# Performance work log

Hardware: AMD Instinct MI355X
Metric: run time of the kernel (lower is better)

## Reference

```python
import jax, jax.numpy as jnp
import numpy as np

H = 4  # n_heads in nn.MultiheadAttention
LN_EPS = 1e-5


def _mha_seq1(x_q, x_kv, in_w, in_b, out_w, out_b):
    """torch nn.MultiheadAttention with batch_first and seq_len=1 on q and kv.
    x_q, x_kv: [B, F]. in_w: [3F, F] (packed q/k/v), out_w: [F, F].
    With a single kv position, softmax over the kv axis is identically 1,
    so the output equals out_proj(v); we still compute scores/softmax so the
    math (and zero grads to Wq/Wk) matches torch exactly.
    """
    B, F = x_q.shape
    dh = F // H
    wq, wk, wv = jnp.split(in_w, 3, axis=0)
    bq, bk, bv = jnp.split(in_b, 3, axis=0)
    q = (x_q @ wq.T + bq).reshape(B, H, dh)
    k = (x_kv @ wk.T + bk).reshape(B, H, dh)
    v = (x_kv @ wv.T + bv).reshape(B, H, dh)
    s = jnp.einsum('bhd,bhd->bh', q, k) / jnp.sqrt(jnp.asarray(dh, x_q.dtype))
    w = jax.nn.softmax(s[..., None], axis=-1)  # [B, H, 1] == 1
    o = (w * v).reshape(B, F)
    return o @ out_w.T + out_b


def _layer_norm(x, g, b):
    mu = jnp.mean(x, axis=-1, keepdims=True)
    var = jnp.mean(jnp.square(x - mu), axis=-1, keepdims=True)
    return (x - mu) * jax.lax.rsqrt(var + LN_EPS) * g + b


def setup_inputs() -> dict:
    key = jax.random.key(0)
    B, GD, TD, F = 16384, 1024, 1024, 2048
    ks = jax.random.split(key, 20)
    s = 0.02  # weight init scale
    return {
        'graph_feat': jax.random.normal(ks[0], (B, GD), jnp.float32),
        'temporal_feat': jax.random.normal(ks[1], (B, TD), jnp.float32),
        'gp_w': jax.random.normal(ks[2], (F, GD), jnp.float32) * s,
        'gp_b': jax.random.normal(ks[3], (F,), jnp.float32) * s,
        'tp_w': jax.random.normal(ks[4], (F, TD), jnp.float32) * s,
        'tp_b': jax.random.normal(ks[5], (F,), jnp.float32) * s,
        'in1_w': jax.random.normal(ks[6], (3 * F, F), jnp.float32) * s,
        'in1_b': jax.random.normal(ks[7], (3 * F,), jnp.float32) * s,
        'out1_w': jax.random.normal(ks[8], (F, F), jnp.float32) * s,
        'out1_b': jax.random.normal(ks[9], (F,), jnp.float32) * s,
        'in2_w': jax.random.normal(ks[10], (3 * F, F), jnp.float32) * s,
        'in2_b': jax.random.normal(ks[11], (3 * F,), jnp.float32) * s,
        'out2_w': jax.random.normal(ks[12], (F, F), jnp.float32) * s,
        'out2_b': jax.random.normal(ks[13], (F,), jnp.float32) * s,
        'gate_w': jax.random.normal(ks[14], (F, 2 * F), jnp.float32) * s,
        'gate_b': jax.random.normal(ks[15], (F,), jnp.float32) * s,
        'ln_g': jnp.ones((F,), jnp.float32),
        'ln_b': jnp.zeros((F,), jnp.float32),
        'lin_w': jax.random.normal(ks[16], (F, F), jnp.float32) * s,
        'lin_b': jax.random.normal(ks[17], (F,), jnp.float32) * s,
    }


def reference(graph_feat, temporal_feat, gp_w, gp_b, tp_w, tp_b,
              in1_w, in1_b, out1_w, out1_b, in2_w, in2_b, out2_w, out2_b,
              gate_w, gate_b, ln_g, ln_b, lin_w, lin_b):
    g = graph_feat @ gp_w.T + gp_b          # [B, F]
    t = temporal_feat @ tp_w.T + tp_b       # [B, F]
    attn1 = _mha_seq1(g, t, in1_w, in1_b, out1_w, out1_b)  # cross1(g, t, t)
    attn2 = _mha_seq1(t, g, in2_w, in2_b, out2_w, out2_b)  # cross2(t, g, g)
    cross = attn1 + attn2
    gate = jax.nn.sigmoid(jnp.concatenate([g, cross], axis=-1) @ gate_w.T + gate_b)
    fused = gate * g + (1.0 - gate) * cross
    fused = _layer_norm(fused + g, ln_g, ln_b)
    return fused @ lin_w.T + lin_b
```

## Files before the change

### kernel.cpp

```cpp
#include <hip/hip_runtime.h>
#include <stdint.h>

typedef __attribute__((ext_vector_type(8))) short short8;
typedef __attribute__((ext_vector_type(4))) float f32x4;

__device__ __forceinline__ unsigned short f2bf(float f) {
  union { float f; uint32_t u; } v; v.f = f;
  uint32_t u = v.u;
  u += 0x7FFF + ((u >> 16) & 1);
  return (unsigned short)(u >> 16);
}
__device__ __forceinline__ float bf2f(unsigned short h) {
  union { uint32_t u; float f; } v; v.u = ((uint32_t)h) << 16;
  return v.f;
}

__global__ void conv_kernel(const float* __restrict__ in,
                            unsigned short* __restrict__ out, int n) {
  long i = ((long)blockIdx.x * blockDim.x + threadIdx.x) * 8;
  if (i >= n) return;
  float4 a = *(const float4*)(in + i);
  float4 b = *(const float4*)(in + i + 4);
  short8 s;
  s[0] = (short)f2bf(a.x); s[1] = (short)f2bf(a.y);
  s[2] = (short)f2bf(a.z); s[3] = (short)f2bf(a.w);
  s[4] = (short)f2bf(b.x); s[5] = (short)f2bf(b.y);
  s[6] = (short)f2bf(b.z); s[7] = (short)f2bf(b.w);
  *(short8*)(out + i) = s;
}

__global__ void convcat_kernel(const float* __restrict__ in,
                               unsigned short* __restrict__ out,
                               int colbase, int n) {
  long i = ((long)blockIdx.x * blockDim.x + threadIdx.x) * 8;
  if (i >= n) return;
  float4 a = *(const float4*)(in + i);
  float4 b = *(const float4*)(in + i + 4);
  short8 s;
  s[0] = (short)f2bf(a.x); s[1] = (short)f2bf(a.y);
  s[2] = (short)f2bf(a.z); s[3] = (short)f2bf(a.w);
  s[4] = (short)f2bf(b.x); s[5] = (short)f2bf(b.y);
  s[6] = (short)f2bf(b.z); s[7] = (short)f2bf(b.w);
  long row = i >> 10, col = i & 1023;
  *(short8*)(out + row * 2048 + colbase + col) = s;
}

__global__ void convs_kernel(const float* __restrict__ in,
                             const float* __restrict__ scale,
                             unsigned short* __restrict__ out, int n) {
  long i = ((long)blockIdx.x * blockDim.x + threadIdx.x) * 8;
  if (i >= n) return;
  short8 s;
#pragma unroll
  for (int j = 0; j < 8; ++j)
    s[j] = (short)f2bf(in[i + j] * scale[(i + j) & 2047]);
  *(short8*)(out + i) = s;
}

__global__ void tconv_kernel(const float* __restrict__ in, int R, int C,
                             unsigned short* __restrict__ out) {
  __shared__ float tile[32][33];
  int c0 = blockIdx.x * 32, r0 = blockIdx.y * 32;
  int tx = threadIdx.x, ty = threadIdx.y;
#pragma unroll
  for (int i = 0; i < 32; i += 8)
    tile[ty + i][tx] = in[(long)(r0 + ty + i) * C + c0 + tx];
  __syncthreads();
#pragma unroll
  for (int i = 0; i < 32; i += 8)
    out[(long)(c0 + ty + i) * R + r0 + tx] = f2bf(tile[tx][ty + i]);
}

enum { CE_PLAIN = 0, CE_WT = 1, CE_ACC = 2 };

template <int CE>
__global__ __launch_bounds__(256)
void compose_kernel(const unsigned short* __restrict__ A, int lda,
                    const unsigned short* __restrict__ W, int ldw,
                    unsigned short* C, int ldc,
                    unsigned short* Ct, long ctoff,
                    int K, int nmt,
                    int pairBase, long aoff, long woff, long coff) {
  constexpr int BK = 32;
  __shared__ unsigned short sA[128 * BK];
  __shared__ unsigned short sB[128 * BK];
  const int tid  = threadIdx.x;
  const int lane = tid & 63;
  const int wave = tid >> 6;
  const int wr = (wave >> 1) * 64;
  const int wc = (wave & 1) * 64;

  int bid = blockIdx.x;
  if (bid >= pairBase) {
    bid -= pairBase;
    A += aoff; W += woff; C += coff; Ct += ctoff;
  }
  const long tileM = (long)(bid % nmt) * 128;
  const long tileN = (long)(bid / nmt) * 128;

  const unsigned short* gA = A + (tileM + (tid >> 2)) * (long)lda + (tid & 3) * 8;
  const unsigned short* gB = W + (tileN + (tid >> 2)) * (long)ldw + (tid & 3) * 8;
  unsigned short* lA = sA + wave * 512;
  unsigned short* lB = sB + wave * 512;

  f32x4 acc[4][4] = {};
  const int fr = lane & 15;
  const int kb = (lane >> 4) * 8;

  for (int k0 = 0; k0 < K; k0 += BK) {
    __builtin_amdgcn_global_load_lds(
        (const __attribute__((address_space(1))) void*)(gA + k0),
        (__attribute__((address_space(3))) void*)(lA), 16, 0, 0);
    __builtin_amdgcn_global_load_lds(
        (const __attribute__((address_space(1))) void*)(gA + k0 + 64 * (long)lda),
        (__attribute__((address_space(3))) void*)(lA + 2048), 16, 0, 0);
    __builtin_amdgcn_global_load_lds(
        (const __attribute__((address_space(1))) void*)(gB + k0),
        (__attribute__((address_space(3))) void*)(lB), 16, 0, 0);
    __builtin_amdgcn_global_load_lds(
        (const __attribute__((address_space(1))) void*)(gB + k0 + 64 * (long)ldw),
        (__attribute__((address_space(3))) void*)(lB + 2048), 16, 0, 0);
    __syncthreads();

    short8 aF[4], bF[4];
#pragma unroll
    for (int m = 0; m < 4; ++m)
      aF[m] = *(const short8*)&sA[(wr + m * 16 + fr) * BK + kb];
#pragma unroll
    for (int n = 0; n < 4; ++n)
      bF[n] = *(const short8*)&sB[(wc + n * 16 + fr) * BK + kb];
#pragma unroll
    for (int m = 0; m < 4; ++m)
#pragma unroll
      for (int n = 0; n < 4; ++n)
        acc[m][n] = __builtin_amdgcn_mfma_f32_16x16x32_bf16(aF[m], bF[n], acc[m][n], 0, 0, 0);
    __syncthreads();
  }

  const int cr = (lane >> 4) * 4;
  const int cc = lane & 15;
#pragma unroll
  for (int m = 0; m < 4; ++m) {
    long r0 = tileM + wr + m * 16 + cr;
#pragma unroll
    for (int n = 0; n < 4; ++n) {
      long c = tileN + wc + n * 16 + cc;
#pragma unroll
      for (int r = 0; r < 4; ++r) {
        long idx = (r0 + r) * (long)ldc + c;
        float v = acc[m][n][r];
        if constexpr (CE == CE_ACC) v += bf2f(C[idx]);
        unsigned short bv = f2bf(v);
        C[idx] = bv;
        if constexpr (CE == CE_WT) Ct[c * 2048 + (r0 + r)] = bv;
      }
    }
  }
}

enum { EPI_BIAS = 0, EPI_LNF32 = 4 };

#define VMW(N) asm volatile("s_waitcnt vmcnt(" #N ")" ::: "memory")
#define SBAR() __builtin_amdgcn_s_barrier()
#define SCB() __builtin_amdgcn_sched_barrier(0)

#define STG(D, OP, HALF, PTR, LD8)                                            \
  { char* lp_ = (char*)smem + ((D)*65536 + (OP)*32768 + (HALF)*16384 + w*2048); \
    __builtin_amdgcn_global_load_lds(                                         \
        (const __attribute__((address_space(1))) void*)(PTR),                 \
        (__attribute__((address_space(3))) void*)lp_, 16, 0, 0);              \
    __builtin_amdgcn_global_load_lds(                                         \
        (const __attribute__((address_space(1))) void*)((PTR) + (LD8)),       \
        (__attribute__((address_space(3))) void*)(lp_ + 1024), 16, 0, 0);     \
    (PTR) += 64; }
#define NOSTG ((void)0)

#define RDA(D, KK) ((KK) ? ((D) ? pA11 : pA01) : ((D) ? pA10 : pA00))
#define RDB(D, KK) ((KK) ? ((D) ? pB11 : pB01) : ((D) ? pB10 : pB00))

template <int EPI, int SWZ>
__global__ __launch_bounds__(512, 2)
void gemm8p_kernel(const unsigned short* __restrict__ A, int lda,
                   const unsigned short* __restrict__ W, int ldw,
                   int K, int ldc, int nmt,
                   const float* __restrict__ bias,
                   const float* __restrict__ bias2,
                   const float2* __restrict__ stats,
                   void* Cv) {
  __shared__ unsigned short smem[65536];

  const int tid = threadIdx.x, lane = tid & 63, w = tid >> 6;
  const int wm = w >> 2, wn = w & 3;

  int bid = blockIdx.x;
  int mt, nt;
  if (SWZ) {
    const int xcd = bid & 7, seq = bid >> 3;
    nt = seq >> 3;
    mt = xcd * 8 + (seq & 7);
  } else {
    mt = bid % nmt;
    nt = bid / nmt;
  }
  const long tileM = (long)mt * 256, tileN = (long)nt * 256;

  const int sRow = w * 16 + (lane >> 3);
  const int sCol = (((lane & 7) ^ ((lane >> 3) & 7)) * 8);
  const unsigned short* pSA0 = A + (tileM + sRow) * (long)lda + sCol;
  const unsigned short* pSA1 = pSA0 + 128 * (long)lda;
  const unsigned short* pSB0 = W + (tileN + sRow) * (long)ldw + sCol;
  const unsigned short* pSB1 = pSB0 + 128 * (long)ldw;
  const long lda8 = 8 * (long)lda, ldw8 = 8 * (long)ldw;

  const int fr = lane & 15, kc = lane >> 4, l7 = lane & 7;
  const char* pA00 = (const char*)smem + (wm * 16 + fr) * 128 + ((kc) ^ l7) * 16;
  const char* pA01 = (const char*)smem + (wm * 16 + fr) * 128 + ((4 + kc) ^ l7) * 16;
  const char* pA10 = pA00 + 65536;
  const char* pA11 = pA01 + 65536;
  const char* pB00 = (const char*)smem + 32768 + (wn * 16 + fr) * 128 + ((kc) ^ l7) * 16;
  const char* pB01 = (const char*)smem + 32768 + (wn * 16 + fr) * 128 + ((4 + kc) ^ l7) * 16;
  const char* pB10 = pB00 + 65536;
  const char* pB11 = pB01 + 65536;

  f32x4 acc[8][4] = {};
  short8 aH[4][2];
  short8 bqS[2][2][2];

#define MPHASE(D, MQ, LB, STGX)                                               \
  {                                                                           \
    _Pragma("unroll") for (int mi = 0; mi < 2; ++mi) {                        \
      aH[mi][0] = *(const short8*)(RDA(D, 0) + (MQ)*16384 + mi * 4096);       \
      aH[mi][1] = *(const short8*)(RDA(D, 1) + (MQ)*16384 + mi * 4096);       \
    }                                                                         \
    if (LB) {                                                                 \
      _Pragma("unroll") for (int q = 0; q < 2; ++q)                           \
      _Pragma("unroll") for (int ni = 0; ni < 2; ++ni) {                      \
        bqS[q][ni][0] = *(const short8*)(RDB(D, 0) + q * 16384 + ni * 8192);  \
        bqS[q][ni][1] = *(const short8*)(RDB(D, 1) + q * 16384 + ni * 8192);  \
      }                                                                       \
    }                                                                         \
    _Pragma("unroll") for (int mi = 2; mi < 4; ++mi) {                        \
      aH[mi][0] = *(const short8*)(RDA(D, 0) + (MQ)*16384 + mi * 4096);       \
      aH[mi][1] = *(const short8*)(RDA(D, 1) + (MQ)*16384 + mi * 4096);       \
    }                                                                         \
    STGX;                                                                     \
    __builtin_amdgcn_s_setprio(1);                                            \
    _Pragma("unroll") for (int mi = 0; mi < 4; ++mi)                          \
    _Pragma("unroll") for (int n = 0; n < 4; ++n) {                           \
      acc[(MQ)*4+mi][n] = __builtin_amdgcn_mfma_f32_16x16x32_bf16(            \
          aH[mi][0], bqS[n >> 1][n & 1][0], acc[(MQ)*4+mi][n], 0, 0, 0);      \
      acc[(MQ)*4+mi][n] = __builtin_amdgcn_mfma_f32_16x16x32_bf16(            \
          aH[mi][1], bqS[n >> 1][n & 1][1], acc[(MQ)*4+mi][n], 0, 0, 0);      \
    }                                                                         \
    __builtin_amdgcn_s_setprio(0);                                            \
    SCB();                                                                    \
  }

  STG(0, 0, 0, pSA0, lda8);
  STG(0, 1, 0, pSB0, ldw8);
  STG(0, 1, 1, pSB1, ldw8);
  STG(0, 0, 1, pSA1, lda8);
  STG(1, 0, 0, pSA0, lda8);
  STG(1, 1, 0, pSB0, ldw8);
  STG(1, 1, 1, pSB1, ldw8);
  VMW(8);
  SBAR();

  const int NIT = K / 128;
  for (int it = 0; it < NIT - 1; ++it) {
    MPHASE(0, 0, 1, STG(1, 0, 1, pSA1, lda8));            VMW(8); SBAR();
    MPHASE(0, 1, 0, STG(0, 0, 0, pSA0, lda8);
                    STG(0, 1, 0, pSB0, ldw8);
                    STG(0, 1, 1, pSB1, ldw8));            VMW(8); SBAR();
    MPHASE(1, 0, 1, STG(0, 0, 1, pSA1, lda8));            VMW(8); SBAR();
    MPHASE(1, 1, 0, STG(1, 0, 0, pSA0, lda8);
                    STG(1, 1, 0, pSB0, ldw8);
                    STG(1, 1, 1, pSB1, ldw8));            VMW(8); SBAR();
  }
  {
    MPHASE(0, 0, 1, STG(1, 0, 1, pSA1, lda8)); VMW(8); SBAR();
    MPHASE(0, 1, 0, NOSTG);                    VMW(2); SBAR();
    MPHASE(1, 0, 1, NOSTG);                    VMW(0); SBAR();
    MPHASE(1, 1, 0, NOSTG);
  }
#undef MPHASE

  const int cr = (lane >> 4) * 4;
  const int cc = lane & 15;
#pragma unroll
  for (int m = 0; m < 8; ++m) {
    long rr = tileM + (m >> 2) * 128 + (m & 3) * 32 + wm * 16 + cr;
#pragma unroll
    for (int n = 0; n < 4; ++n) {
      long c = tileN + (n >> 1) * 128 + (n & 1) * 64 + wn * 16 + cc;
      float b1 = bias ? bias[c] : 0.0f;
      float b2 = bias2 ? bias2[c] : 0.0f;
#pragma unroll
      for (int r = 0; r < 4; ++r) {
        long row = rr + r;
        long idx = row * (long)ldc + c;
        float v = acc[m][n][r];
        if constexpr (EPI == EPI_BIAS) {
          ((unsigned short*)Cv)[idx] = f2bf(v + b1 + b2);
        }
        if constexpr (EPI == EPI_LNF32) {
          float2 st = stats[row];
          ((float*)Cv)[idx] = v * st.y - st.y * st.x * b1 + b2;
        }
      }
    }
  }
}

__global__ __launch_bounds__(256) void fusestats_kernel(
    const unsigned short* __restrict__ CL, const unsigned short* __restrict__ G,
    unsigned short* __restrict__ PL, float2* __restrict__ stats) {
  const int row = blockIdx.x;
  const int t = threadIdx.x, lane = t & 63, wave = t >> 6;
  short8 xc = *(const short8*)&CL[(long)row * 4096 + t * 8];
  short8 xl = *(const short8*)&CL[(long)row * 4096 + 2048 + t * 8];
  short8 xg = *(const short8*)&G[(long)row * 2048 + t * 8];
  short8 o8;
  float s = 0.f, s2 = 0.f;
#pragma unroll
  for (int j = 0; j < 8; ++j) {
    float cv = bf2f((unsigned short)xc[j]);
    float lv = bf2f((unsigned short)xl[j]);
    float gv = bf2f((unsigned short)xg[j]);
    float gt = 1.0f / (1.0f + expf(-lv));
    unsigned short pb = f2bf(gt * gv + (1.0f - gt) * cv + gv);
    o8[j] = (short)pb;
    float x = bf2f(pb);
    s += x; s2 += x * x;
  }
  *(short8*)(PL + (long)row * 2048 + t * 8) = o8;
#pragma unroll
  for (int off = 1; off < 64; off <<= 1) {
    s  += __shfl_xor(s, off);
    s2 += __shfl_xor(s2, off);
  }
  __shared__ float red[8];
  if (lane == 0) { red[wave] = s; red[4 + wave] = s2; }
  __syncthreads();
  if (t == 0) {
    float ts  = red[0] + red[1] + red[2] + red[3];
    float ts2 = red[4] + red[5] + red[6] + red[7];
    float mean = ts * (1.0f / 2048.0f);
    float var  = ts2 * (1.0f / 2048.0f) - mean * mean;
    stats[row] = make_float2(mean, rsqrtf(var + 1e-5f));
  }
}

__device__ __forceinline__ float blkRed(float s, float* red, int lane, int wave) {
#pragma unroll
  for (int off = 1; off < 64; off <<= 1) s += __shfl_xor(s, off);
  if (lane == 0) red[wave] = s;
  __syncthreads();
  return red[0] + red[1] + red[2] + red[3];
}

__global__ __launch_bounds__(256) void biascompP_kernel(
    const unsigned short* __restrict__ wO1b, const unsigned short* __restrict__ wO2b,
    const unsigned short* __restrict__ Wc1, const unsigned short* __restrict__ Wc2,
    const float* __restrict__ bv1, const float* __restrict__ bv2,
    const float* __restrict__ tpb, const float* __restrict__ gpb,
    const float* __restrict__ o1b, const float* __restrict__ o2b,
    float* __restrict__ bcV) {
  __shared__ float red[4];
  int c = blockIdx.x, t = threadIdx.x, lane = t & 63, wave = t >> 6;
  int k = t * 8;
  float s = 0.f;
  short8 a1 = *(const short8*)(wO1b + (long)c * 2048 + k);
  short8 a2 = *(const short8*)(wO2b + (long)c * 2048 + k);
  short8 a3 = *(const short8*)(Wc1 + (long)c * 2048 + k);
  short8 a4 = *(const short8*)(Wc2 + (long)c * 2048 + k);
#pragma unroll
  for (int j = 0; j < 8; ++j)
    s += bf2f((unsigned short)a1[j]) * bv1[k + j]
       + bf2f((unsigned short)a2[j]) * bv2[k + j]
       + bf2f((unsigned short)a3[j]) * tpb[k + j]
       + bf2f((unsigned short)a4[j]) * gpb[k + j];
  float tot = blkRed(s, red, lane, wave);
  if (t == 0) bcV[c] = tot + o1b[c] + o2b[c];
}

__global__ __launch_bounds__(256) void bgateP_kernel(
    const float* __restrict__ gate_w, const float* __restrict__ gate_b,
    const float* __restrict__ gpb, const float* __restrict__ bcV,
    float* __restrict__ bgateV) {
  __shared__ float red[4];
  int n = blockIdx.x, t = threadIdx.x, lane = t & 63, wave = t >> 6;
  const float* row = gate_w + (long)n * 4096;
  float s = 0.f;
  int k = t * 8;
#pragma unroll
  for (int j = 0; j < 8; ++j)
    s += row[k + j] * gpb[k + j] + row[2048 + k + j] * bcV[k + j];
  float tot = blkRed(s, red, lane, wave);
  if (t == 0) bgateV[n] = tot + gate_b[n];
}

__global__ __launch_bounds__(256) void uvP_kernel(
    const unsigned short* __restrict__ wlinp, const float* __restrict__ lin_w,
    const float* __restrict__ ln_beta, const float* __restrict__ lin_b,
    float* __restrict__ uV, float* __restrict__ vV) {
  __shared__ float redu[4], redv[4];
  int n = blockIdx.x, t = threadIdx.x, lane = t & 63, wave = t >> 6;
  int k = t * 8;
  short8 a1 = *(const short8*)(wlinp + (long)n * 2048 + k);
  float u = 0.f, v = 0.f;
#pragma unroll
  for (int j = 0; j < 8; ++j) {
    u += bf2f((unsigned short)a1[j]);
    v += ln_beta[k + j] * lin_w[(long)n * 2048 + k + j];
  }
#pragma unroll
  for (int off = 1; off < 64; off <<= 1) {
    u += __shfl_xor(u, off);
    v += __shfl_xor(v, off);
  }
  if (lane == 0) { redu[wave] = u; redv[wave] = v; }
  __syncthreads();
  if (t == 0) {
    uV[n] = redu[0] + redu[1] + redu[2] + redu[3];
    vV[n] = redv[0] + redv[1] + redv[2] + redv[3] + lin_b[n];
  }
}

extern "C" void kernel_launch(void* const* d_in, const int* in_sizes, int n_in,
                              void* d_out, int out_size, void* d_ws, size_t ws_size,
                              hipStream_t stream) {
  const float* graph    = (const float*)d_in[0];
  const float* temporal = (const float*)d_in[1];
  const float* gp_w  = (const float*)d_in[2];
  const float* gp_b  = (const float*)d_in[3];
  const float* tp_w  = (const float*)d_in[4];
  const float* tp_b  = (const float*)d_in[5];
  const float* in1_w = (const float*)d_in[6];
  const float* in1_b = (const float*)d_in[7];
  const float* out1_w = (const float*)d_in[8];
  const float* out1_b = (const float*)d_in[9];
  const float* in2_w = (const float*)d_in[10];
  const float* in2_b = (const float*)d_in[11];
  const float* out2_w = (const float*)d_in[12];
  const float* out2_b = (const float*)d_in[13];
  const float* gate_w = (const float*)d_in[14];
  const float* gate_b = (const float*)d_in[15];
  const float* ln_g  = (const float*)d_in[16];
  const float* ln_b  = (const float*)d_in[17];
  const float* lin_w = (const float*)d_in[18];
  const float* lin_b = (const float*)d_in[19];

  const int Bm = 16384, F = 2048, GD = 1024;
  const long BF = (long)Bm * F, FF = (long)F * F, FG = (long)F * GD;

  unsigned short* TG   = (unsigned short*)d_ws;
  unsigned short* PL   = TG;
  unsigned short* Gbuf = TG + BF;
  unsigned short* wLIN = Gbuf + BF;
  unsigned short* wGP  = wLIN + FF;
  unsigned short* Wcg  = wGP + FG;
  unsigned short* Wcross = Wcg;
  unsigned short* Wgate  = Wcg + FF;
  float* bc2V   = (float*)(Wcg + 2 * FF);
  float* uV     = bc2V + 2 * F;
  float* vV     = uV + F;
  float2* stats = (float2*)(vV + F);

  unsigned short* DO      = (unsigned short*)d_out;
  unsigned short* wv1T    = DO;
  unsigned short* wv2T    = wv1T + FF;
  unsigned short* tpT     = wv2T + FF;
  unsigned short* gpT     = tpT + FG;
  unsigned short* Wc1     = gpT + FG;
  unsigned short* Wc2     = Wc1 + FF;
  unsigned short* wO1b    = Wc2 + FF;
  unsigned short* wO2b    = wO1b + FF;
  unsigned short* wGATEb  = wO2b + FF;
  unsigned short* WcrossT = wGATEb + 2 * FF;
  unsigned short* CL      = DO;

  auto conv = [&](const float* src, unsigned short* dst, long n) {
    conv_kernel<<<dim3((unsigned)(n / 8 / 256)), 256, 0, stream>>>(src, dst, (int)n);
  };
  convcat_kernel<<<dim3((unsigned)(Bm * GD / 8 / 256)), 256, 0, stream>>>(
      temporal, TG, 0, Bm * GD);
  convcat_kernel<<<dim3((unsigned)(Bm * GD / 8 / 256)), 256, 0, stream>>>(
      graph, TG, GD, Bm * GD);
  conv(gp_w, wGP, FG);
  conv(out1_w, wO1b, FF);
  conv(out2_w, wO2b, FF);
  conv(gate_w, wGATEb, 2 * FF);
  convs_kernel<<<dim3((unsigned)(FF / 8 / 256)), 256, 0, stream>>>(lin_w, ln_g, wLIN, (int)FF);
  tconv_kernel<<<dim3(F / 32, F / 32), dim3(32, 8), 0, stream>>>(in1_w + 2 * FF, F, F, wv1T);
  tconv_kernel<<<dim3(F / 32, F / 32), dim3(32, 8), 0, stream>>>(in2_w + 2 * FF, F, F, wv2T);
  tconv_kernel<<<dim3(GD / 32, F / 32), dim3(32, 8), 0, stream>>>(tp_w, F, GD, tpT);
  tconv_kernel<<<dim3(GD / 32, F / 32), dim3(32, 8), 0, stream>>>(gp_w, F, GD, gpT);

  compose_kernel<CE_PLAIN><<<dim3(512), dim3(256), 0, stream>>>(
      wO1b, F, wv1T, F, Wc1, F, nullptr, 0, F, 16,
      256, wO2b - wO1b, wv2T - wv1T, Wc2 - Wc1);
  compose_kernel<CE_WT><<<dim3(256), dim3(256), 0, stream>>>(
      Wc1, F, tpT, F, Wcross, F, WcrossT, (long)1024 * 2048, F, 16,
      128, Wc2 - Wc1, gpT - tpT, 1024);
  biascompP_kernel<<<dim3(F), dim3(256), 0, stream>>>(
      wO1b, wO2b, Wc1, Wc2, in1_b + 2 * F, in2_b + 2 * F, tp_b, gp_b,
      out1_b, out2_b, bc2V);
  compose_kernel<CE_PLAIN><<<dim3(256), dim3(256), 0, stream>>>(
      wGATEb + F, 2 * F, WcrossT, F, Wgate, F, nullptr, 0, F, 16,
      1 << 30, 0, 0, 0);
  compose_kernel<CE_ACC><<<dim3(128), dim3(256), 0, stream>>>(
      wGATEb, 2 * F, gpT, F, Wgate + GD, F, nullptr, 0, F, 16,
      1 << 30, 0, 0, 0);
  bgateP_kernel<<<dim3(F), dim3(256), 0, stream>>>(gate_w, gate_b, gp_b, bc2V,
                                                   bc2V + F);
  uvP_kernel<<<dim3(F), dim3(256), 0, stream>>>(wLIN, lin_w, ln_b, lin_b, uV, vV);

  dim3 blk(512);
  gemm8p_kernel<EPI_BIAS, 1><<<dim3(512), blk, 0, stream>>>(
      TG + GD, F, wGP, GD, GD, F, 0,
      gp_b, nullptr, nullptr, Gbuf);
  gemm8p_kernel<EPI_BIAS, 1><<<dim3(1024), blk, 0, stream>>>(
      TG, F, Wcg, F, F, 2 * F, 0,
      bc2V, nullptr, nullptr, CL);
  fusestats_kernel<<<dim3(Bm), dim3(256), 0, stream>>>(CL, Gbuf, PL, stats);
  gemm8p_kernel<EPI_LNF32, 1><<<dim3(512), blk, 0, stream>>>(
      PL, F, wLIN, F, F, F, 0,
      uV, vV, stats, (void*)d_out);
}
```

Baseline: 818.5 us.

## Replace 256x256 phased GEMM with simpler 128x128 double-buffered GEMM kernel

Swaps the 256x256-tile, 8-phase pipelined bf16 MFMA GEMM for a 128x128-tile kernel with a simple two-stage LDS double buffer and a 64-deep K step. Launch bounds rise to 4 blocks per CU and shared memory is halved to allow more concurrent blocks, with an XCD-aware tile mapping parameterized by the number of M tiles. The aim is higher occupancy and simpler scheduling. In exchange, per-tile data reuse drops and each iteration waits for all outstanding global loads before the barrier, which can expose memory latency.

```diff
diff --git a/kernel.cpp b/kernel.cpp
--- a/kernel.cpp
+++ b/kernel.cpp
@@ -162,137 +162,107 @@
 
 #define VMW(N) asm volatile("s_waitcnt vmcnt(" #N ")" ::: "memory")
 #define SBAR() __builtin_amdgcn_s_barrier()
-#define SCB() __builtin_amdgcn_sched_barrier(0)
-
-#define STG(D, OP, HALF, PTR, LD8)                                            \
-  { char* lp_ = (char*)smem + ((D)*65536 + (OP)*32768 + (HALF)*16384 + w*2048); \
-    __builtin_amdgcn_global_load_lds(                                         \
-        (const __attribute__((address_space(1))) void*)(PTR),                 \
-        (__attribute__((address_space(3))) void*)lp_, 16, 0, 0);              \
-    __builtin_amdgcn_global_load_lds(                                         \
-        (const __attribute__((address_space(1))) void*)((PTR) + (LD8)),       \
-        (__attribute__((address_space(3))) void*)(lp_ + 1024), 16, 0, 0);     \
-    (PTR) += 64; }
-#define NOSTG ((void)0)
-
-#define RDA(D, KK) ((KK) ? ((D) ? pA11 : pA01) : ((D) ? pA10 : pA00))
-#define RDB(D, KK) ((KK) ? ((D) ? pB11 : pB01) : ((D) ? pB10 : pB00))
-
-template <int EPI, int SWZ>
-__global__ __launch_bounds__(512, 2)
-void gemm8p_kernel(const unsigned short* __restrict__ A, int lda,
-                   const unsigned short* __restrict__ W, int ldw,
-                   int K, int ldc, int nmt,
-                   const float* __restrict__ bias,
-                   const float* __restrict__ bias2,
-                   const float2* __restrict__ stats,
-                   void* Cv) {
-  __shared__ unsigned short smem[65536];
+
+template <int EPI>
+__global__ __launch_bounds__(512, 4)
+void gemm128_kernel(const unsigned short* __restrict__ A, int lda,
+                    const unsigned short* __restrict__ W, int ldw,
+                    int K, int ldc, int nmt,
+                    const float* __restrict__ bias,
+                    const float* __restrict__ bias2,
+                    const float2* __restrict__ stats,
+                    void* Cv) {
+  __shared__ unsigned short smem[32768];
 
   const int tid = threadIdx.x, lane = tid & 63, w = tid >> 6;
   const int wm = w >> 2, wn = w & 3;
 
-  int bid = blockIdx.x;
-  int mt, nt;
-  if (SWZ) {
-    const int xcd = bid & 7, seq = bid >> 3;
-    nt = seq >> 3;
-    mt = xcd * 8 + (seq & 7);
-  } else {
-    mt = bid % nmt;
-    nt = bid / nmt;
-  }
-  const long tileM = (long)mt * 256, tileN = (long)nt * 256;
+  const int q = nmt >> 3;
+  const int xcd = blockIdx.x & 7, seq = blockIdx.x >> 3;
+  const int mt = xcd * q + (seq % q);
+  const int nt = seq / q;
+  const long tileM = (long)mt * 128, tileN = (long)nt * 128;
 
   const int sRow = w * 16 + (lane >> 3);
   const int sCol = (((lane & 7) ^ ((lane >> 3) & 7)) * 8);
-  const unsigned short* pSA0 = A + (tileM + sRow) * (long)lda + sCol;
-  const unsigned short* pSA1 = pSA0 + 128 * (long)lda;
-  const unsigned short* pSB0 = W + (tileN + sRow) * (long)ldw + sCol;
-  const unsigned short* pSB1 = pSB0 + 128 * (long)ldw;
+  const unsigned short* pSA = A + (tileM + sRow) * (long)lda + sCol;
+  const unsigned short* pSB = W + (tileN + sRow) * (long)ldw + sCol;
   const long lda8 = 8 * (long)lda, ldw8 = 8 * (long)ldw;
 
   const int fr = lane & 15, kc = lane >> 4, l7 = lane & 7;
-  const char* pA00 = (const char*)smem + (wm * 16 + fr) * 128 + ((kc) ^ l7) * 16;
-  const char* pA01 = (const char*)smem + (wm * 16 + fr) * 128 + ((4 + kc) ^ l7) * 16;
-  const char* pA10 = pA00 + 65536;
-  const char* pA11 = pA01 + 65536;
-  const char* pB00 = (const char*)smem + 32768 + (wn * 16 + fr) * 128 + ((kc) ^ l7) * 16;
-  const char* pB01 = (const char*)smem + 32768 + (wn * 16 + fr) * 128 + ((4 + kc) ^ l7) * 16;
-  const char* pB10 = pB00 + 65536;
-  const char* pB11 = pB01 + 65536;
-
-  f32x4 acc[8][4] = {};
-  short8 aH[4][2];
-  short8 bqS[2][2][2];
-
-#define MPHASE(D, MQ, LB, STGX)                                               \
+  const unsigned aOff0 = (wm * 64 + fr) * 128 + ((kc) ^ l7) * 16;
+  const unsigned aOff1 = (wm * 64 + fr) * 128 + ((4 + kc) ^ l7) * 16;
+  const unsigned bOff0 = 16384 + (wn * 32 + fr) * 128 + ((kc) ^ l7) * 16;
+  const unsigned bOff1 = 16384 + (wn * 32 + fr) * 128 + ((4 + kc) ^ l7) * 16;
+
+  f32x4 acc[4][2] = {};
+
+#define STGK(D)                                                               \
+  { char* la_ = (char*)smem + (D) * 32768 + w * 2048;                         \
+    char* lb_ = la_ + 16384;                                                  \
+    __builtin_amdgcn_global_load_lds(                                         \
+        (const __attribute__((address_space(1))) void*)pSA,                   \
+        (__attribute__((address_space(3))) void*)la_, 16, 0, 0);              \
+    __builtin_amdgcn_global_load_lds(                                         \
+        (const __attribute__((address_space(1))) void*)(pSA + lda8),          \
+        (__attribute__((address_space(3))) void*)(la_ + 1024), 16, 0, 0);     \
+    __builtin_amdgcn_global_load_lds(                                         \
+        (const __attribute__((address_space(1))) void*)pSB,                   \
+        (__attribute__((address_space(3))) void*)lb_, 16, 0, 0);              \
+    __builtin_amdgcn_global_load_lds(                                         \
+        (const __attribute__((address_space(1))) void*)(pSB + ldw8),          \
+        (__attribute__((address_space(3))) void*)(lb_ + 1024), 16, 0, 0);     \
+    pSA += 64; pSB += 64; }
+
+#define ITER(D, LAST)                                                         \
   {                                                                           \
-    _Pragma("unroll") for (int mi = 0; mi < 2; ++mi) {                        \
-      aH[mi][0] = *(const short8*)(RDA(D, 0) + (MQ)*16384 + mi * 4096);       \
-      aH[mi][1] = *(const short8*)(RDA(D, 1) + (MQ)*16384 + mi * 4096);       \
+    if (!(LAST)) STGK((D) ^ 1);                                               \
+    short8 aF[4][2], bF[2][2];                                                \
+    const char* ba = (const char*)smem + (D) * 32768;                         \
+    _Pragma("unroll") for (int m = 0; m < 4; ++m) {                           \
+      aF[m][0] = *(const short8*)(ba + aOff0 + m * 2048);                     \
+      aF[m][1] = *(const short8*)(ba + aOff1 + m * 2048);                     \
     }                                                                         \
-    if (LB) {                                                                 \
-      _Pragma("unroll") for (int q = 0; q < 2; ++q)                           \
-      _Pragma("unroll") for (int ni = 0; ni < 2; ++ni) {                      \
-        bqS[q][ni][0] = *(const short8*)(RDB(D, 0) + q * 16384 + ni * 8192);  \
-        bqS[q][ni][1] = *(const short8*)(RDB(D, 1) + q * 16384 + ni * 8192);  \
-      }                                                                       \
+    _Pragma("unroll") for (int n = 0; n < 2; ++n) {                           \
+      bF[n][0] = *(const short8*)(ba + bOff0 + n * 2048);                     \
+      bF[n][1] = *(const short8*)(ba + bOff1 + n * 2048);                     \
     }                                                                         \
-    _Pragma("unroll") for (int mi = 2; mi < 4; ++mi) {                        \
-      aH[mi][0] = *(const short8*)(RDA(D, 0) + (MQ)*16384 + mi * 4096);       \
-      aH[mi][1] = *(const short8*)(RDA(D, 1) + (MQ)*16384 + mi * 4096);       \
-    }                                                                         \
-    STGX;                                                                     \
     __builtin_amdgcn_s_setprio(1);                                            \
-    _Pragma("unroll") for (int mi = 0; mi < 4; ++mi)                          \
-    _Pragma("unroll") for (int n = 0; n < 4; ++n) {                           \
-      acc[(MQ)*4+mi][n] = __builtin_amdgcn_mfma_f32_16x16x32_bf16(            \
-          aH[mi][0], bqS[n >> 1][n & 1][0], acc[(MQ)*4+mi][n], 0, 0, 0);      \
-      acc[(MQ)*4+mi][n] = __builtin_amdgcn_mfma_f32_16x16x32_bf16(            \
-          aH[mi][1], bqS[n >> 1][n & 1][1], acc[(MQ)*4+mi][n], 0, 0, 0);      \
+    _Pragma("unroll") for (int m = 0; m < 4; ++m)                             \
+    _Pragma("unroll") for (int n = 0; n < 2; ++n) {                           \
+      acc[m][n] = __builtin_amdgcn_mfma_f32_16x16x32_bf16(                    \
+          aF[m][0], bF[n][0], acc[m][n], 0, 0, 0);                            \
+      acc[m][n] = __builtin_amdgcn_mfma_f32_16x16x32_bf16(                    \
+          aF[m][1], bF[n][1], acc[m][n], 0, 0, 0);                            \
     }                                                                         \
     __builtin_amdgcn_s_setprio(0);                                            \
-    SCB();                                                                    \
-  }
-
-  STG(0, 0, 0, pSA0, lda8);
-  STG(0, 1, 0, pSB0, ldw8);
-  STG(0, 1, 1, pSB1, ldw8);
-  STG(0, 0, 1, pSA1, lda8);
-  STG(1, 0, 0, pSA0, lda8);
-  STG(1, 1, 0, pSB0, ldw8);
-  STG(1, 1, 1, pSB1, ldw8);
-  VMW(8);
+    asm volatile("s_waitcnt lgkmcnt(0)" ::: "memory");                        \
+    if (!(LAST)) VMW(0);                                                      \
+    SBAR();                                                                   \
+  }
+
+  STGK(0);
+  VMW(0);
   SBAR();
 
-  const int NIT = K / 128;
-  for (int it = 0; it < NIT - 1; ++it) {
-    MPHASE(0, 0, 1, STG(1, 0, 1, pSA1, lda8));            VMW(8); SBAR();
-    MPHASE(0, 1, 0, STG(0, 0, 0, pSA0, lda8);
-                    STG(0, 1, 0, pSB0, ldw8);
-                    STG(0, 1, 1, pSB1, ldw8));            VMW(8); SBAR();
-    MPHASE(1, 0, 1, STG(0, 0, 1, pSA1, lda8));            VMW(8); SBAR();
-    MPHASE(1, 1, 0, STG(1, 0, 0, pSA0, lda8);
-                    STG(1, 1, 0, pSB0, ldw8);
-                    STG(1, 1, 1, pSB1, ldw8));            VMW(8); SBAR();
-  }
-  {
-    MPHASE(0, 0, 1, STG(1, 0, 1, pSA1, lda8)); VMW(8); SBAR();
-    MPHASE(0, 1, 0, NOSTG);                    VMW(2); SBAR();
-    MPHASE(1, 0, 1, NOSTG);                    VMW(0); SBAR();
-    MPHASE(1, 1, 0, NOSTG);
-  }
-#undef MPHASE
+  const int NT = K / 64;
+  for (int kt = 0; kt < NT - 2; kt += 2) {
+    ITER(0, 0);
+    ITER(1, 0);
+  }
+  ITER(0, 0);
+  ITER(1, 1);
+#undef ITER
+#undef STGK
 
   const int cr = (lane >> 4) * 4;
   const int cc = lane & 15;
 #pragma unroll
-  for (int m = 0; m < 8; ++m) {
-    long rr = tileM + (m >> 2) * 128 + (m & 3) * 32 + wm * 16 + cr;
-#pragma unroll
-    for (int n = 0; n < 4; ++n) {
-      long c = tileN + (n >> 1) * 128 + (n & 1) * 64 + wn * 16 + cc;
+  for (int m = 0; m < 4; ++m) {
+    long rr = tileM + wm * 64 + m * 16 + cr;
+#pragma unroll
+    for (int n = 0; n < 2; ++n) {
+      long c = tileN + wn * 32 + n * 16 + cc;
       float b1 = bias ? bias[c] : 0.0f;
       float b2 = bias2 ? bias2[c] : 0.0f;
 #pragma unroll
@@ -517,14 +487,15 @@
   uvP_kernel<<<dim3(F), dim3(256), 0, stream>>>(wLIN, lin_w, ln_b, lin_b, uV, vV);
 
   dim3 blk(512);
-  gemm8p_kernel<EPI_BIAS, 1><<<dim3(512), blk, 0, stream>>>(
-      TG + GD, F, wGP, GD, GD, F, 0,
+  const int NMT = Bm / 128;
+  gemm128_kernel<EPI_BIAS><<<dim3(NMT * (F / 128)), blk, 0, stream>>>(
+      TG + GD, F, wGP, GD, GD, F, NMT,
       gp_b, nullptr, nullptr, Gbuf);
-  gemm8p_kernel<EPI_BIAS, 1><<<dim3(1024), blk, 0, stream>>>(
-      TG, F, Wcg, F, F, 2 * F, 0,
+  gemm128_kernel<EPI_BIAS><<<dim3(NMT * (2 * F / 128)), blk, 0, stream>>>(
+      TG, F, Wcg, F, F, 2 * F, NMT,
       bc2V, nullptr, nullptr, CL);
   fusestats_kernel<<<dim3(Bm), dim3(256), 0, stream>>>(CL, Gbuf, PL, stats);
-  gemm8p_kernel<EPI_LNF32, 1><<<dim3(512), blk, 0, stream>>>(
-      PL, F, wLIN, F, F, F, 0,
+  gemm128_kernel<EPI_LNF32><<<dim3(NMT * (F / 128)), blk, 0, stream>>>(
+      PL, F, wLIN, F, F, F, NMT,
       uV, vV, stats, (void*)d_out);
 }
```

New measurement: 911.6 us. 11.4% more time.
